# Optimization experiments

Measured on AMD Instinct MI355X. Metric: run time of the kernel, lower is better.

## Reference

```python
import jax, jax.numpy as jnp
import numpy as np

B, T, D_IN, D_H, D_OUT = 32, 2048, 1024, 1024, 1024

def setup_inputs() -> dict:
    key = jax.random.key(0)
    k1, k2, k3, k4, k5 = jax.random.split(key, 5)
    s = jax.random.normal(k1, (B, D_IN), dtype=jnp.float32)
    h = jax.random.normal(k2, (B, T, D_H), dtype=jnp.float32)
    # params (original uses np.random.random, i.e. uniform [0,1); scale kept modest)
    W_a = jax.random.uniform(k3, (D_IN, D_OUT), dtype=jnp.float32)
    U_a = jax.random.uniform(k4, (D_H, D_OUT), dtype=jnp.float32)
    v_a = jax.random.uniform(k5, (D_OUT,), dtype=jnp.float32)
    return {"s": s, "h": h, "W_a": W_a, "U_a": U_a, "v_a": v_a}

def reference(s, h, W_a, U_a, v_a):
    # Bahdanau additive attention:
    # e_bt = v_a . tanh(s W_a + h_t U_a);  a = softmax_t(e);  c_b = sum_t a_bt h_bt
    u_a_h = jnp.einsum('bth,ho->bto', h, U_a)            # [B,T,O]
    w_a_s = jnp.einsum('bi,io->bo', s, W_a)[:, None, :]  # [B,1,O]
    e = jnp.einsum('bto,o->bt', jnp.tanh(w_a_s + u_a_h), v_a)  # [B,T]
    a = jax.nn.softmax(e, axis=-1)                       # [B,T]
    c = jnp.einsum('bt,bth->bh', a, h)                   # [B,H]
    return c
```

## Files before the change

kernel.cpp:

```cpp
#include <hip/hip_runtime.h>
#include <hip/hip_bf16.h>
#include <stdint.h>

#define Bb 32
#define Tt 2048
#define Dd 1024

typedef float    f32x4 __attribute__((ext_vector_type(4)));
typedef _Float16 f16x8 __attribute__((ext_vector_type(8)));
typedef uint32_t u32;

#define WS_A     131072
#define WS_EP    393216
#define WS_UT    4587520

__device__ __forceinline__ void gll16(const void* g, const void* lds) {
  __builtin_amdgcn_global_load_lds(
      (const __attribute__((address_space(1))) u32*)(uintptr_t)g,
      (__attribute__((address_space(3))) u32*)(uint32_t)(uintptr_t)lds,
      16, 0, 0);
}

__global__ __launch_bounds__(256) void k_ws(const float* __restrict__ s,
                                            const float* __restrict__ W,
                                            float* __restrict__ w2_ws) {
  const int b = blockIdx.x >> 2;
  const int o = (blockIdx.x & 3) * 256 + threadIdx.x;
  __shared__ float s_sh[Dd];
#pragma unroll
  for (int j = 0; j < 4; ++j)
    s_sh[threadIdx.x + 256 * j] = s[b * Dd + threadIdx.x + 256 * j];
  __syncthreads();
  float acc = 0.f;
#pragma unroll 8
  for (int i = 0; i < Dd; ++i) acc += s_sh[i] * W[(size_t)i * Dd + o];
  w2_ws[b * Dd + o] = 2.f * acc;
}

__global__ __launch_bounds__(256) void k_ut(const float* __restrict__ U,
                                            uint8_t* __restrict__ U_ts) {
  const int i0 = (blockIdx.x >> 4) * 64;
  const int o0 = (blockIdx.x & 15) * 64;
  __shared__ float tile[64][65];
  const int tx = threadIdx.x & 63;
  const int ty = threadIdx.x >> 6;
#pragma unroll
  for (int jj = 0; jj < 16; ++jj)
    tile[tx][ty + 4 * jj] = U[(size_t)(i0 + ty + 4 * jj) * Dd + o0 + tx];
  __syncthreads();
#pragma unroll
  for (int it = 0; it < 2; ++it) {
    const int g  = it * 256 + threadIdx.x;
    const int ol = g & 63;
    const int kg = g >> 6;
    const int o  = o0 + ol;
    const int k  = i0 + kg * 8;
    f16x8 r;
#pragma unroll
    for (int m = 0; m < 8; ++m) r[m] = (_Float16)tile[ol][kg * 8 + m];
    const int ob  = o >> 7, ks = k >> 6;
    const int o_l = o & 127, k_l = k & 63;
    const size_t byte = ((size_t)(ob * 16 + ks) << 14)
                      + (size_t)((k_l >> 5) * 8192 + (o_l >> 6) * 4096
                      + ((o_l >> 4) & 3) * 1024
                      + (((k_l >> 3) & 3) * 16 + (o_l & 15)) * 16);
    *(f16x8*)(U_ts + byte) = r;
  }
}

__global__ __launch_bounds__(512, 3) void k_e(const float* __restrict__ h,
                                              const uint8_t* __restrict__ U_ts,
                                              const float* __restrict__ w2_ws,
                                              const float* __restrict__ v_a,
                                              float* __restrict__ e_part) {
  const int blk = blockIdx.x;
  const int b   = blk >> 6;
  const int obb = (blk >> 4) & 3;
  const int tb  = blk & 15;
  const int tid  = threadIdx.x;
  const int lane = tid & 63;
  const int w    = tid >> 6;
  const int tw   = w >> 2;
  const int ow   = w & 3;

  __shared__ __align__(16) uint8_t Al[32768];
  __shared__ __align__(16) uint8_t Bl[16384];
  __shared__ float exch[512];

  const uint8_t* Asrc[4];
#pragma unroll
  for (int q = 0; q < 4; ++q)
    Asrc[q] = U_ts + ((size_t)((obb * 2 + (q >> 1)) * 16) << 14)
            + (size_t)(((q & 1) * 512 + w * 64 + lane) * 16);

  const float* hb[2];
  int baddr[2];
#pragma unroll
  for (int j = 0; j < 2; ++j) {
    const int u   = j * 512 + tid;
    const int t_l = u >> 3;
    const int kg  = u & 7;
    hb[j] = h + ((size_t)(b * Tt + tb * 128 + t_l)) * Dd + kg * 8;
    const int kk  = kg >> 2;
    const int klo = kg & 3;
    baddr[j] = kk * 8192 + (t_l >> 6) * 4096 + ((t_l >> 4) & 3) * 1024
             + (klo * 16 + ((t_l & 15) ^ kg)) * 16;
  }

  const int aoff = (ow >> 1) * 16384 + (ow & 1) * 4096 + lane * 16;
  const int klo_r = lane >> 4;
  const int rs0 = (klo_r * 16 + ((lane & 15) ^ klo_r)) * 16;
  const int rs1 = (klo_r * 16 + ((lane & 15) ^ klo_r ^ 4)) * 16;
  const int boff = tw * 4096;

  f32x4 acc[4][4] = {};
  f32x4 br[4];
  f16x8 pk[2];

#pragma unroll
  for (int j = 0; j < 2; ++j) {
    br[2 * j]     = *(const f32x4*)(hb[j]);
    br[2 * j + 1] = *(const f32x4*)(hb[j] + 4);
  }
#pragma unroll
  for (int j = 0; j < 2; ++j) {
    f16x8 t;
#pragma unroll
    for (int m2 = 0; m2 < 4; ++m2) {
      t[m2]     = (_Float16)br[2 * j][m2];
      t[4 + m2] = (_Float16)br[2 * j + 1][m2];
    }
    pk[j] = t;
  }

#pragma unroll 1
  for (int ks = 0; ks < 16; ++ks) {
    __syncthreads();
#pragma unroll
    for (int q = 0; q < 4; ++q)
      gll16(Asrc[q] + ((size_t)ks << 14), Al + q * 8192 + w * 1024);
#pragma unroll
    for (int j = 0; j < 2; ++j) *(f16x8*)(Bl + baddr[j]) = pk[j];
    __syncthreads();
    const int kso = (ks < 15 ? ks + 1 : 0) * 64;
#pragma unroll
    for (int j = 0; j < 2; ++j) {
      br[2 * j]     = *(const f32x4*)(hb[j] + kso);
      br[2 * j + 1] = *(const f32x4*)(hb[j] + kso + 4);
    }
#pragma unroll
    for (int kk = 0; kk < 2; ++kk) {
      f16x8 af[4], bf[4];
#pragma unroll
      for (int n = 0; n < 4; ++n)
        af[n] = *(const f16x8*)(Al + aoff + kk * 8192 + n * 1024);
#pragma unroll
      for (int m = 0; m < 4; ++m)
        bf[m] = *(const f16x8*)(Bl + boff + kk * 8192 + m * 1024 + (kk ? rs1 : rs0));
#pragma unroll
      for (int m = 0; m < 4; ++m)
#pragma unroll
        for (int n = 0; n < 4; ++n)
          acc[m][n] = __builtin_amdgcn_mfma_f32_16x16x32_f16(af[n], bf[m],
                                                             acc[m][n], 0, 0, 0);
    }
#pragma unroll
    for (int j = 0; j < 2; ++j) {
      f16x8 t;
#pragma unroll
      for (int m2 = 0; m2 < 4; ++m2) {
        t[m2]     = (_Float16)br[2 * j][m2];
        t[4 + m2] = (_Float16)br[2 * j + 1][m2];
      }
      pk[j] = t;
    }
  }

  const float* wbase = w2_ws + b * Dd + obb * 256;
  const float* vbase = v_a + obb * 256;
  float ep[4] = {0.f, 0.f, 0.f, 0.f};
#pragma unroll
  for (int n = 0; n < 4; ++n) {
    const int og = ow * 64 + n * 16 + ((lane >> 4) << 2);
    const f32x4 w4 = *(const f32x4*)(wbase + og);
    const f32x4 v4 = *(const f32x4*)(vbase + og);
#pragma unroll
    for (int m = 0; m < 4; ++m)
#pragma unroll
      for (int r = 0; r < 4; ++r) {
        const float x = __builtin_fmaf(acc[m][n][r], 2.f, w4[r]);
        ep[m] += v4[r] * (1.f - 2.f / (__expf(x) + 1.f));
      }
  }
#pragma unroll
  for (int m = 0; m < 4; ++m) {
    ep[m] += __shfl_xor(ep[m], 16, 64);
    ep[m] += __shfl_xor(ep[m], 32, 64);
  }
  __syncthreads();
  if (lane < 16) {
#pragma unroll
    for (int m = 0; m < 4; ++m)
      exch[ow * 128 + tw * 64 + m * 16 + lane] = ep[m];
  }
  __syncthreads();
  if (tid < 128) {
    const float sv = exch[tid] + exch[128 + tid] + exch[256 + tid] + exch[384 + tid];
    e_part[((size_t)(obb * Bb + b)) * Tt + tb * 128 + tid] = sv;
  }
}

__global__ __launch_bounds__(256) void k_sm(const float* __restrict__ e_part,
                                            float* __restrict__ a_ws) {
  const int b = blockIdx.x;
  const int lane = threadIdx.x & 63;
  const int wv = threadIdx.x >> 6;
  __shared__ float red[8];
  float ev[8];
  float m = -1e30f;
#pragma unroll
  for (int j = 0; j < 8; ++j) {
    const int t = threadIdx.x + 256 * j;
    float sv = 0.f;
#pragma unroll
    for (int o = 0; o < 4; ++o) sv += e_part[((size_t)(o * Bb + b)) * Tt + t];
    ev[j] = sv;
    m = fmaxf(m, sv);
  }
#pragma unroll
  for (int sft = 1; sft < 64; sft <<= 1) m = fmaxf(m, __shfl_xor(m, sft, 64));
  if (lane == 0) red[wv] = m;
  __syncthreads();
  m = fmaxf(fmaxf(red[0], red[1]), fmaxf(red[2], red[3]));
  float sum = 0.f;
#pragma unroll
  for (int j = 0; j < 8; ++j) { ev[j] = __expf(ev[j] - m); sum += ev[j]; }
#pragma unroll
  for (int sft = 1; sft < 64; sft <<= 1) sum += __shfl_xor(sum, sft, 64);
  if (lane == 0) red[4 + wv] = sum;
  __syncthreads();
  const float inv = 1.f / (red[4] + red[5] + red[6] + red[7]);
#pragma unroll
  for (int j = 0; j < 8; ++j) a_ws[b * Tt + threadIdx.x + 256 * j] = ev[j] * inv;
}

__global__ __launch_bounds__(256) void k_c1(const float* __restrict__ h,
                                            const float* __restrict__ a_ws,
                                            float* __restrict__ cpart) {
  const int b  = blockIdx.x >> 5;
  const int tc = blockIdx.x & 31;
  const int t0 = tc << 6;
  __shared__ float a_sh[64];
  if (threadIdx.x < 64) a_sh[threadIdx.x] = a_ws[b * Tt + t0 + threadIdx.x];
  __syncthreads();
  f32x4 acc = {0.f, 0.f, 0.f, 0.f};
  const float* hb = h + ((size_t)b * Tt + t0) * Dd + threadIdx.x * 4;
#pragma unroll 4
  for (int t = 0; t < 64; ++t) {
    const f32x4 hv = *(const f32x4*)(hb + (size_t)t * Dd);
    acc += a_sh[t] * hv;
  }
  *(f32x4*)(cpart + ((size_t)(tc * 32 + b) << 10) + threadIdx.x * 4) = acc;
}

__global__ __launch_bounds__(256) void k_c2(const float* __restrict__ cpart,
                                            float* __restrict__ out) {
  const int gid = blockIdx.x * 256 + threadIdx.x;
  const int b = gid >> 10;
  const int d = gid & 1023;
  float sv = 0.f;
#pragma unroll
  for (int tc = 0; tc < 32; ++tc) sv += cpart[((size_t)(tc * 32 + b) << 10) + d];
  out[gid] = sv;
}

extern "C" void kernel_launch(void* const* d_in, const int* in_sizes, int n_in,
                              void* d_out, int out_size, void* d_ws, size_t ws_size,
                              hipStream_t stream) {
  (void)in_sizes; (void)n_in; (void)out_size; (void)ws_size;
  const float* s  = (const float*)d_in[0];
  const float* h  = (const float*)d_in[1];
  const float* W  = (const float*)d_in[2];
  const float* U  = (const float*)d_in[3];
  const float* v  = (const float*)d_in[4];
  uint8_t* ws = (uint8_t*)d_ws;
  float*   w2_ws  = (float*)ws;
  float*   a_ws   = (float*)(ws + WS_A);
  float*   e_part = (float*)(ws + WS_EP);
  float*   cpart  = (float*)(ws + WS_EP);
  uint8_t* U_ts   = ws + WS_UT;

  k_ws<<<128, 256, 0, stream>>>(s, W, w2_ws);
  k_ut<<<256, 256, 0, stream>>>(U, U_ts);
  k_e <<<2048, 512, 0, stream>>>(h, U_ts, w2_ws, v, e_part);
  k_sm<<<Bb, 256, 0, stream>>>(e_part, a_ws);
  k_c1<<<1024, 256, 0, stream>>>(h, a_ws, cpart);
  k_c2<<<128, 256, 0, stream>>>(cpart, (float*)d_out);
}
```

Measured before the change: 283.0 us.

## Double-buffer LDS tiles in k_e with single barrier per K-step

The main GEMM loop of k_e now uses double-buffered LDS for the U tile and the h tile. Each iteration prefetches the next tile via global_load_lds and writes the converted h registers into the other buffer, while MFMAs run on the current buffer. Only one barrier per iteration remains, synchronised with explicit waitcnt and sched_barrier, and s_setprio raises wave priority around the MFMA bursts. The larger LDS footprint lowers the occupancy target from 3 to 2 blocks per CU, and the hand-placed waitcnts risk subtle hazards.

```diff
diff --git a/kernel.cpp b/kernel.cpp
--- a/kernel.cpp
+++ b/kernel.cpp
@@ -68,7 +68,7 @@
   }
 }
 
-__global__ __launch_bounds__(512, 3) void k_e(const float* __restrict__ h,
+__global__ __launch_bounds__(512, 2) void k_e(const float* __restrict__ h,
                                               const uint8_t* __restrict__ U_ts,
                                               const float* __restrict__ w2_ws,
                                               const float* __restrict__ v_a,
@@ -83,8 +83,8 @@
   const int tw   = w >> 2;
   const int ow   = w & 3;
 
-  __shared__ __align__(16) uint8_t Al[32768];
-  __shared__ __align__(16) uint8_t Bl[16384];
+  __shared__ __align__(16) uint8_t Al[2][32768];
+  __shared__ __align__(16) uint8_t Bl[2][16384];
   __shared__ float exch[512];
 
   const uint8_t* Asrc[4];
@@ -123,6 +123,9 @@
     br[2 * j + 1] = *(const f32x4*)(hb[j] + 4);
   }
 #pragma unroll
+  for (int q = 0; q < 4; ++q)
+    gll16(Asrc[q], &Al[0][0] + q * 8192 + w * 1024);
+#pragma unroll
   for (int j = 0; j < 2; ++j) {
     f16x8 t;
 #pragma unroll
@@ -131,38 +134,29 @@
       t[4 + m2] = (_Float16)br[2 * j + 1][m2];
     }
     pk[j] = t;
-  }
+    *(f16x8*)(&Bl[0][0] + baddr[j]) = t;
+  }
+#pragma unroll
+  for (int j = 0; j < 2; ++j) {
+    br[2 * j]     = *(const f32x4*)(hb[j] + 64);
+    br[2 * j + 1] = *(const f32x4*)(hb[j] + 64 + 4);
+  }
+  asm volatile("s_waitcnt lgkmcnt(0)" ::: "memory");
+  __builtin_amdgcn_sched_barrier(0);
 
 #pragma unroll 1
   for (int ks = 0; ks < 16; ++ks) {
-    __syncthreads();
-#pragma unroll
-    for (int q = 0; q < 4; ++q)
-      gll16(Asrc[q] + ((size_t)ks << 14), Al + q * 8192 + w * 1024);
-#pragma unroll
-    for (int j = 0; j < 2; ++j) *(f16x8*)(Bl + baddr[j]) = pk[j];
-    __syncthreads();
-    const int kso = (ks < 15 ? ks + 1 : 0) * 64;
-#pragma unroll
-    for (int j = 0; j < 2; ++j) {
-      br[2 * j]     = *(const f32x4*)(hb[j] + kso);
-      br[2 * j + 1] = *(const f32x4*)(hb[j] + kso + 4);
-    }
-#pragma unroll
-    for (int kk = 0; kk < 2; ++kk) {
-      f16x8 af[4], bf[4];
-#pragma unroll
-      for (int n = 0; n < 4; ++n)
-        af[n] = *(const f16x8*)(Al + aoff + kk * 8192 + n * 1024);
-#pragma unroll
-      for (int m = 0; m < 4; ++m)
-        bf[m] = *(const f16x8*)(Bl + boff + kk * 8192 + m * 1024 + (kk ? rs1 : rs0));
-#pragma unroll
-      for (int m = 0; m < 4; ++m)
-#pragma unroll
-        for (int n = 0; n < 4; ++n)
-          acc[m][n] = __builtin_amdgcn_mfma_f32_16x16x32_f16(af[n], bf[m],
-                                                             acc[m][n], 0, 0, 0);
+    const int cur = ks & 1;
+    const int nxt = cur ^ 1;
+    asm volatile("s_waitcnt vmcnt(4)" ::: "memory");
+    __builtin_amdgcn_sched_barrier(0);
+    __builtin_amdgcn_s_barrier();
+    __builtin_amdgcn_sched_barrier(0);
+    {
+      const size_t ko = (size_t)((ks + 1) & 15) << 14;
+#pragma unroll
+      for (int q = 0; q < 4; ++q)
+        gll16(Asrc[q] + ko, &Al[nxt][0] + q * 8192 + w * 1024);
     }
 #pragma unroll
     for (int j = 0; j < 2; ++j) {
@@ -173,6 +167,54 @@
         t[4 + m2] = (_Float16)br[2 * j + 1][m2];
       }
       pk[j] = t;
+      *(f16x8*)(&Bl[nxt][0] + baddr[j]) = t;
+    }
+    {
+      const int kso = ((ks + 2) & 15) * 64;
+#pragma unroll
+      for (int j = 0; j < 2; ++j) {
+        br[2 * j]     = *(const f32x4*)(hb[j] + kso);
+        br[2 * j + 1] = *(const f32x4*)(hb[j] + kso + 4);
+      }
+    }
+    __builtin_amdgcn_sched_barrier(0);
+    {
+      f16x8 af[4], bf[4];
+#pragma unroll
+      for (int n = 0; n < 4; ++n)
+        af[n] = *(const f16x8*)(&Al[cur][0] + aoff + n * 1024);
+#pragma unroll
+      for (int m = 0; m < 4; ++m)
+        bf[m] = *(const f16x8*)(&Bl[cur][0] + boff + m * 1024 + rs0);
+      asm volatile("s_waitcnt lgkmcnt(0)" ::: "memory");
+      __builtin_amdgcn_sched_barrier(0);
+      __builtin_amdgcn_s_setprio(1);
+#pragma unroll
+      for (int m = 0; m < 4; ++m)
+#pragma unroll
+        for (int n = 0; n < 4; ++n)
+          acc[m][n] = __builtin_amdgcn_mfma_f32_16x16x32_f16(af[n], bf[m],
+                                                             acc[m][n], 0, 0, 0);
+      __builtin_amdgcn_s_setprio(0);
+    }
+    {
+      f16x8 af[4], bf[4];
+#pragma unroll
+      for (int n = 0; n < 4; ++n)
+        af[n] = *(const f16x8*)(&Al[cur][0] + aoff + 8192 + n * 1024);
+#pragma unroll
+      for (int m = 0; m < 4; ++m)
+        bf[m] = *(const f16x8*)(&Bl[cur][0] + boff + 8192 + m * 1024 + rs1);
+      asm volatile("s_waitcnt lgkmcnt(0)" ::: "memory");
+      __builtin_amdgcn_sched_barrier(0);
+      __builtin_amdgcn_s_setprio(1);
+#pragma unroll
+      for (int m = 0; m < 4; ++m)
+#pragma unroll
+        for (int n = 0; n < 4; ++n)
+          acc[m][n] = __builtin_amdgcn_mfma_f32_16x16x32_f16(af[n], bf[m],
+                                                             acc[m][n], 0, 0, 0);
+      __builtin_amdgcn_s_setprio(0);
     }
   }
 
```

Result: slower. 316.4 us (+11.8%).
